# Optimization experiments

Measured on AMD Instinct MI355X. Metric: run time of the kernel, lower is better.

Reference implementation:

```python
import jax, jax.numpy as jnp
import numpy as np

DT = 0.001  # fixed dt in SimplifiedSSM.forward
LN_EPS = 1e-5


def _layernorm(x, g, b):
    m = jnp.mean(x, axis=-1, keepdims=True)
    v = jnp.mean(jnp.square(x - m), axis=-1, keepdims=True)
    return (x - m) * jax.lax.rsqrt(v + LN_EPS) * g + b


def setup_inputs() -> dict:
    key = jax.random.key(0)
    ks = jax.random.split(key, 12)
    Bn, C, H, W = 8, 1024, 32, 32
    depth, S = 4, 128
    d = C
    inp = {
        "x": jax.random.normal(ks[0], (Bn, C, H, W), dtype=jnp.float32),
        # SSM params, stacked over depth. A scaled by 0.1 for numerical stability
        # of the length-1024 recurrence (same math, tamer eigenvalues).
        "A": 0.1 * jax.random.normal(ks[1], (depth, S, S), dtype=jnp.float32),
        "Bp": jax.random.normal(ks[2], (depth, S, d), dtype=jnp.float32),
        "Cp": jax.random.normal(ks[3], (depth, d, S), dtype=jnp.float32),
        "Dp": jax.random.normal(ks[4], (depth, d), dtype=jnp.float32),
        # Linear layers (PyTorch convention: y = x @ W.T + b)
        "Wi": jax.random.normal(ks[5], (depth, d, d), dtype=jnp.float32) / np.sqrt(d),
        "bi": jax.random.normal(ks[6], (depth, d), dtype=jnp.float32) * 0.01,
        "Wo": jax.random.normal(ks[7], (depth, d, d), dtype=jnp.float32) / np.sqrt(d),
        "bo": jax.random.normal(ks[8], (depth, d), dtype=jnp.float32) * 0.01,
        # LayerNorm affine params
        "gamma": jnp.ones((depth, d), dtype=jnp.float32),
        "beta": jnp.zeros((depth, d), dtype=jnp.float32),
    }
    return inp


def reference(x, A, Bp, Cp, Dp, Wi, bi, Wo, bo, gamma, beta):
    Bn, C, H, W = x.shape
    depth, S, _ = A.shape
    # b c h w -> b (h w) c
    seq = x.reshape(Bn, C, H * W).transpose(0, 2, 1)
    eye = jnp.eye(S, dtype=x.dtype)
    for i in range(depth):
        n = _layernorm(seq, gamma[i], beta[i])
        u = n @ Wi[i].T + bi[i]                       # (B, L, d)
        A_bar = eye + DT * A[i]                       # (S, S)
        ub = jnp.einsum('bld,sd->lbs', u, DT * Bp[i]) # (L, B, S)

        def step(h, ub_t):
            h = h @ A_bar.T + ub_t
            return h, h

        h0 = jnp.zeros((Bn, S), dtype=x.dtype)
        _, hs = jax.lax.scan(step, h0, ub)            # hs: (L, B, S)
        y = jnp.einsum('lbs,ds->bld', hs, Cp[i]) + u * Dp[i]
        seq = seq + y @ Wo[i].T + bo[i]
    return seq.transpose(0, 2, 1).reshape(Bn, C, H, W)
```

## Files before the change

kernel.cpp:

```cpp
#include <hip/hip_runtime.h>
#include <stdint.h>

#define DT_STEP 0.001f
#define LN_EPS  1e-5f
#define Bn      8
#define Lseq    1024
#define Dm      1024
#define Sn      128
#define DEPTH   4
#define Mrows   (Bn * Lseq)
#define Qc      32
#define NCHUNK  (Lseq / Qc)
#define NPOW    33

typedef short bf16x8 __attribute__((ext_vector_type(8)));
typedef float f32x4  __attribute__((ext_vector_type(4)));

__device__ __forceinline__ unsigned short f2bf(float f) {
    unsigned int u = __float_as_uint(f);
    u += 0x7fffu + ((u >> 16) & 1u);
    return (unsigned short)(u >> 16);
}

#define GLOAD_LDS16(gp, lp)                                                \
    __builtin_amdgcn_global_load_lds(                                      \
        (const __attribute__((address_space(1))) unsigned int*)(gp),       \
        (__attribute__((address_space(3))) unsigned int*)(lp), 16, 0, 0)

__global__ __launch_bounds__(256) void f2bf_kernel(const float* __restrict__ src,
                                                   unsigned short* __restrict__ dst,
                                                   int n) {
    int i = (blockIdx.x * 256 + threadIdx.x) * 4;
    if (i < n) {
        float4 v = *(const float4*)(src + i);
        ushort4 o;
        o.x = f2bf(v.x); o.y = f2bf(v.y); o.z = f2bf(v.z); o.w = f2bf(v.w);
        *(ushort4*)(dst + i) = o;
    }
}

__global__ __launch_bounds__(256) void convscale_kernel(const float* __restrict__ Wo,
                                                        const float* __restrict__ Dp,
                                                        unsigned short* __restrict__ dst) {
    int z = blockIdx.y;
    int i = (blockIdx.x * 256 + threadIdx.x) * 4;
    const float* S = Wo + (size_t)z * Dm * Dm;
    const float* dp = Dp + (size_t)z * Dm;
    float4 v = *(const float4*)(S + i);
    int c = i & (Dm - 1);
    float4 d = *(const float4*)(dp + c);
    ushort4 o;
    o.x = f2bf(v.x * d.x); o.y = f2bf(v.y * d.y);
    o.z = f2bf(v.z * d.z); o.w = f2bf(v.w * d.w);
    *(ushort4*)(dst + (size_t)z * Dm * Dm + i) = o;
}

__global__ __launch_bounds__(256) void transpose_f2bf(const float* __restrict__ src,
                                                      unsigned short* __restrict__ dst,
                                                      int R, int C) {
    __shared__ float t[32][33];
    int z = blockIdx.z;
    const float* S = src + (size_t)z * R * C;
    unsigned short* D = dst + (size_t)z * R * C;
    int r0 = blockIdx.y * 32, c0 = blockIdx.x * 32;
    int tx = threadIdx.x & 31, ty = threadIdx.x >> 5;
    for (int rr = ty; rr < 32; rr += 8)
        t[rr][tx] = S[(size_t)(r0 + rr) * C + c0 + tx];
    __syncthreads();
    for (int rr = ty; rr < 32; rr += 8)
        D[(size_t)(c0 + rr) * R + r0 + tx] = f2bf(t[tx][rr]);
}

__global__ __launch_bounds__(256) void c2dt_kernel(const float* __restrict__ Bp,
                                                   const float* __restrict__ bi,
                                                   float* __restrict__ c2dt) {
    int z = blockIdx.x, s = blockIdx.y;
    int tid = threadIdx.x;
    const float* br = Bp + ((size_t)z * Sn + s) * Dm;
    const float* bb = bi + (size_t)z * Dm;
    float4 v = *(const float4*)(br + tid * 4);
    float4 w = *(const float4*)(bb + tid * 4);
    float acc = v.x * w.x + v.y * w.y + v.z * w.z + v.w * w.w;
#pragma unroll
    for (int off = 32; off > 0; off >>= 1) acc += __shfl_down(acc, off, 64);
    __shared__ float red[4];
    if ((tid & 63) == 0) red[tid >> 6] = acc;
    __syncthreads();
    if (tid == 0) c2dt[z * Sn + s] = DT_STEP * (red[0] + red[1] + red[2] + red[3]);
}

__global__ __launch_bounds__(1024) void transpose_bll(const float* __restrict__ src,
                                                      float* __restrict__ dst) {
    __shared__ float tile[32][33];
    int b  = blockIdx.z;
    int i0 = blockIdx.y * 32, j0 = blockIdx.x * 32;
    int tx = threadIdx.x, ty = threadIdx.y;
    const float* S = src + (size_t)b * Dm * Lseq;
    float*       D = dst + (size_t)b * Dm * Lseq;
    tile[ty][tx] = S[(size_t)(j0 + ty) * 1024 + i0 + tx];
    __syncthreads();
    D[(size_t)(i0 + ty) * 1024 + j0 + tx] = tile[tx][ty];
}

__global__ __launch_bounds__(256) void ln_kernel(const float* __restrict__ x,
                                                 unsigned short* __restrict__ outp,
                                                 const float* __restrict__ g,
                                                 const float* __restrict__ bta) {
    int row = blockIdx.x;
    int tid = threadIdx.x;
    const float* xr = x + (size_t)row * Dm;
    float4 v = *(const float4*)(xr + tid * 4);
    float s  = v.x + v.y + v.z + v.w;
    float ss = v.x * v.x + v.y * v.y + v.z * v.z + v.w * v.w;
#pragma unroll
    for (int off = 32; off > 0; off >>= 1) {
        s  += __shfl_down(s, off, 64);
        ss += __shfl_down(ss, off, 64);
    }
    __shared__ float red[8];
    __shared__ float mv[2];
    int wave = tid >> 6, lane = tid & 63;
    if (lane == 0) { red[wave] = s; red[4 + wave] = ss; }
    __syncthreads();
    if (tid == 0) {
        float st  = red[0] + red[1] + red[2] + red[3];
        float sst = red[4] + red[5] + red[6] + red[7];
        float mean = st / (float)Dm;
        float var  = sst / (float)Dm - mean * mean;
        mv[0] = mean;
        mv[1] = rsqrtf(var + LN_EPS);
    }
    __syncthreads();
    float mean = mv[0], rstd = mv[1];
    int c = tid * 4;
    float4 gv = *(const float4*)(g + c);
    float4 bv = *(const float4*)(bta + c);
    ushort4 o;
    o.x = f2bf((v.x - mean) * rstd * gv.x + bv.x);
    o.y = f2bf((v.y - mean) * rstd * gv.y + bv.y);
    o.z = f2bf((v.z - mean) * rstd * gv.z + bv.z);
    o.w = f2bf((v.w - mean) * rstd * gv.w + bv.w);
    *(ushort4*)(outp + (size_t)row * Dm + c) = o;
}

__global__ __launch_bounds__(512) void gemm_bk64(
    const unsigned short* __restrict__ A1, int sA1,
    const unsigned short* __restrict__ A2, int sA2, int KA1,
    const unsigned short* __restrict__ B1, int sB1,
    const unsigned short* __restrict__ B2, int sB2,
    float* __restrict__ Cf, unsigned short* __restrict__ Ch,
    const float* __restrict__ bias1, const float* __restrict__ bias2,
    int ny, int N, int K, float scale, int mode,
    long batchA, long batchB, long batchC) {
    __shared__ __align__(16) unsigned short As[1024 * 8];
    __shared__ __align__(16) unsigned short Bs[1024 * 8];
    int flat = blockIdx.x;
    int rb = flat % ny, cb = flat / ny;
    int row0 = rb * 128, col0 = cb * 128;
    int z = blockIdx.y;
    int tid  = threadIdx.x;
    int wave = tid >> 6, lane = tid & 63;
    int wm = (wave & 1) * 64, wn = (wave >> 1) * 32;
    int lr = lane & 15, lq = lane >> 4;

    int rowS[2], kclS[2], slotOff[2];
#pragma unroll
    for (int q = 0; q < 2; q++) {
        int s = tid + q * 512;
        rowS[q] = s >> 3;
        kclS[q] = (s & 7) ^ ((s >> 3) & 7);
        slotOff[q] = s * 8;
    }
    int aoff[4][2], boff[2][2];
#pragma unroll
    for (int i = 0; i < 4; i++)
#pragma unroll
        for (int h = 0; h < 2; h++) {
            int ra = wm + i * 16 + lr;
            aoff[i][h] = (ra * 8 + ((lq + 4 * h) ^ (ra & 7))) * 8;
        }
#pragma unroll
    for (int j = 0; j < 2; j++)
#pragma unroll
        for (int h = 0; h < 2; h++) {
            int rn = wn + j * 16 + lr;
            boff[j][h] = (rn * 8 + ((lq + 4 * h) ^ (rn & 7))) * 8;
        }

    const unsigned short* A1b = A1 + (size_t)z * batchA;
    const unsigned short* BfixBlk = nullptr;
    int sBfix = sB1;
    if (mode == 0) {
        if (col0 < N - 128) { BfixBlk = B1 + (size_t)col0 * sB1; sBfix = sB1; }
        else                { BfixBlk = B2;                      sBfix = sB2; }
    } else if (mode == 2) {
        BfixBlk = B1 + (size_t)z * batchB + (size_t)col0 * sB1;
        sBfix = sB1;
    }

    f32x4 acc[4][2];
#pragma unroll
    for (int i = 0; i < 4; i++)
#pragma unroll
        for (int j = 0; j < 2; j++) acc[i][j] = (f32x4){0.f, 0.f, 0.f, 0.f};

    for (int k0 = 0; k0 < K; k0 += 64) {
        const unsigned short *Ab, *Bb;
        int sa, sb, ko;
        if (mode == 1) {
            if (k0 < KA1) { Ab = A1; sa = sA1; Bb = B1 + (size_t)col0 * sB1; sb = sB1; ko = k0; }
            else          { Ab = A2; sa = sA2; Bb = B2 + (size_t)col0 * sB2; sb = sB2; ko = k0 - KA1; }
        } else {
            Ab = A1b; sa = sA1; Bb = BfixBlk; sb = sBfix; ko = k0;
        }
        const unsigned short* Abr = Ab + (size_t)row0 * sa + ko;
        const unsigned short* Bbr = Bb + ko;
        __syncthreads();
#pragma unroll
        for (int q = 0; q < 2; q++) {
            GLOAD_LDS16(Abr + (size_t)rowS[q] * sa + kclS[q] * 8, &As[slotOff[q]]);
            GLOAD_LDS16(Bbr + (size_t)rowS[q] * sb + kclS[q] * 8, &Bs[slotOff[q]]);
        }
        __syncthreads();
#pragma unroll
        for (int h = 0; h < 2; h++) {
            bf16x8 af[4], bfr[2];
#pragma unroll
            for (int i = 0; i < 4; i++) af[i]  = *(const bf16x8*)&As[aoff[i][h]];
#pragma unroll
            for (int j = 0; j < 2; j++) bfr[j] = *(const bf16x8*)&Bs[boff[j][h]];
#pragma unroll
            for (int i = 0; i < 4; i++)
#pragma unroll
                for (int j = 0; j < 2; j++)
                    acc[i][j] = __builtin_amdgcn_mfma_f32_16x16x32_bf16(af[i], bfr[j],
                                                                       acc[i][j], 0, 0, 0);
        }
    }
#pragma unroll
    for (int i = 0; i < 4; i++) {
#pragma unroll
        for (int j = 0; j < 2; j++) {
#pragma unroll
            for (int r = 0; r < 4; r++) {
                int row = row0 + wm + i * 16 + lq * 4 + r;
                int col = col0 + wn + j * 16 + lr;
                float v = acc[i][j][r];
                if (mode == 0) {
                    int nu = N - 128;
                    if (col < nu) {
                        Ch[(size_t)row * nu + col] = f2bf(v + bias1[col]);
                    } else {
                        int cc = col - nu;
                        Cf[(size_t)row * 128 + cc] = v + bias2[cc];
                    }
                } else if (mode == 1) {
                    size_t idx = (size_t)row * N + col;
                    Cf[idx] = Cf[idx] + v + bias1[col];
                } else {
                    Ch[(size_t)z * batchC + (size_t)row * N + col] = f2bf(v * scale);
                }
            }
        }
    }
}

__global__ __launch_bounds__(128) void pow_init(const float* __restrict__ Amat,
                                                float* __restrict__ Pow) {
    int i = blockIdx.x;
    int s = blockIdx.y;
    int k = threadIdx.x;
    float eye = (s == k) ? 1.f : 0.f;
    size_t base = (size_t)i * NPOW * (Sn * Sn);
    Pow[base + (size_t)s * Sn + k] = eye;
    Pow[base + (size_t)(Sn * Sn) + (size_t)s * Sn + k] =
        eye + DT_STEP * Amat[(size_t)i * Sn * Sn + (size_t)s * Sn + k];
}

__global__ __launch_bounds__(256) void pow_mul(float* __restrict__ Pow, int m, int kmax) {
    int job = blockIdx.z;
    int i  = job / kmax;
    int kk = job % kmax + 1;
    const float* Pa = Pow + ((size_t)i * NPOW + m) * (Sn * Sn);
    const float* Pb = Pow + ((size_t)i * NPOW + kk) * (Sn * Sn);
    float*       Pc = Pow + ((size_t)i * NPOW + m + kk) * (Sn * Sn);
    int r0 = blockIdx.y * 64, c0 = blockIdx.x * 32;
    __shared__ float Asl[64 * 129];
    __shared__ float Bsl[128 * 32];
    int tx = threadIdx.x, ty = threadIdx.y;
    int tid = ty * 16 + tx;
    for (int idx = tid; idx < 64 * 128; idx += 256) {
        int r = idx >> 7, cc = idx & 127;
        Asl[r * 129 + cc] = Pa[(size_t)(r0 + r) * 128 + cc];
    }
    for (int idx = tid; idx < 128 * 32; idx += 256) {
        int r = idx >> 5, cc = idx & 31;
        Bsl[r * 32 + cc] = Pb[(size_t)r * 128 + c0 + cc];
    }
    __syncthreads();
    float acc[4][2] = {{0.f,0.f},{0.f,0.f},{0.f,0.f},{0.f,0.f}};
    for (int k = 0; k < 128; k++) {
        float b0 = Bsl[k * 32 + tx * 2];
        float b1 = Bsl[k * 32 + tx * 2 + 1];
#pragma unroll
        for (int r = 0; r < 4; r++) {
            float a = Asl[(ty * 4 + r) * 129 + k];
            acc[r][0] += a * b0;
            acc[r][1] += a * b1;
        }
    }
#pragma unroll
    for (int r = 0; r < 4; r++) {
        Pc[(size_t)(r0 + ty * 4 + r) * 128 + c0 + tx * 2]     = acc[r][0];
        Pc[(size_t)(r0 + ty * 4 + r) * 128 + c0 + tx * 2 + 1] = acc[r][1];
    }
}

__global__ __launch_bounds__(128) void local_scan(const float* __restrict__ ub,
                                                  float* __restrict__ hs,
                                                  const float* __restrict__ Abar) {
    int b = blockIdx.x / NCHUNK;
    int c = blockIdx.x % NCHUNK;
    int s = threadIdx.x;
    float arow[Sn];
#pragma unroll
    for (int k = 0; k < Sn; k += 4) {
        float4 v = *(const float4*)(Abar + (size_t)s * Sn + k);
        arow[k] = v.x; arow[k + 1] = v.y; arow[k + 2] = v.z; arow[k + 3] = v.w;
    }
    __shared__ __align__(16) float hsh[Sn];
    hsh[s] = 0.f;
    __syncthreads();
    size_t base = (size_t)(b * Lseq + c * Qc) * Sn + s;
    for (int t = 0; t < Qc; t++) {
        float ut = ub[base + (size_t)t * Sn];
        float a0 = 0.f, a1 = 0.f, a2 = 0.f, a3 = 0.f;
#pragma unroll
        for (int k = 0; k < Sn; k += 16) {
            float4 h0 = *(const float4*)&hsh[k];
            float4 h1 = *(const float4*)&hsh[k + 4];
            float4 h2 = *(const float4*)&hsh[k + 8];
            float4 h3 = *(const float4*)&hsh[k + 12];
            a0 += arow[k + 0] * h0.x + arow[k + 1] * h0.y + arow[k + 2] * h0.z + arow[k + 3] * h0.w;
            a1 += arow[k + 4] * h1.x + arow[k + 5] * h1.y + arow[k + 6] * h1.z + arow[k + 7] * h1.w;
            a2 += arow[k + 8] * h2.x + arow[k + 9] * h2.y + arow[k + 10] * h2.z + arow[k + 11] * h2.w;
            a3 += arow[k + 12] * h3.x + arow[k + 13] * h3.y + arow[k + 14] * h3.z + arow[k + 15] * h3.w;
        }
        float hv = ut + (a0 + a1) + (a2 + a3);
        hs[base + (size_t)t * Sn] = hv;
        __syncthreads();
        hsh[s] = hv;
        __syncthreads();
    }
}

__global__ __launch_bounds__(128) void carry_scan(const float* __restrict__ hs,
                                                  const float* __restrict__ AQ,
                                                  float* __restrict__ carry) {
    int b = blockIdx.x;
    int s = threadIdx.x;
    float le[NCHUNK];
#pragma unroll
    for (int c = 0; c < NCHUNK; c++)
        le[c] = hs[(size_t)(b * Lseq + c * Qc + Qc - 1) * Sn + s];
    float arow[Sn];
#pragma unroll
    for (int k = 0; k < Sn; k += 4) {
        float4 v = *(const float4*)(AQ + (size_t)s * Sn + k);
        arow[k] = v.x; arow[k + 1] = v.y; arow[k + 2] = v.z; arow[k + 3] = v.w;
    }
    __shared__ __align__(16) float csh[Sn];
    csh[s] = 0.f;
    __syncthreads();
    for (int c = 0; c < NCHUNK; c++) {
        carry[((size_t)b * NCHUNK + c) * Sn + s] = csh[s];
        float a0 = 0.f, a1 = 0.f, a2 = 0.f, a3 = 0.f;
#pragma unroll
        for (int k = 0; k < Sn; k += 16) {
            float4 h0 = *(const float4*)&csh[k];
            float4 h1 = *(const float4*)&csh[k + 4];
            float4 h2 = *(const float4*)&csh[k + 8];
            float4 h3 = *(const float4*)&csh[k + 12];
            a0 += arow[k + 0] * h0.x + arow[k + 1] * h0.y + arow[k + 2] * h0.z + arow[k + 3] * h0.w;
            a1 += arow[k + 4] * h1.x + arow[k + 5] * h1.y + arow[k + 6] * h1.z + arow[k + 7] * h1.w;
            a2 += arow[k + 8] * h2.x + arow[k + 9] * h2.y + arow[k + 10] * h2.z + arow[k + 11] * h2.w;
            a3 += arow[k + 12] * h3.x + arow[k + 13] * h3.y + arow[k + 14] * h3.z + arow[k + 15] * h3.w;
        }
        float cv = le[c] + (a0 + a1) + (a2 + a3);
        __syncthreads();
        csh[s] = cv;
        __syncthreads();
    }
}

__global__ __launch_bounds__(256) void fixup_scan(const float* __restrict__ hs,
                                                  unsigned short* __restrict__ hs_bf,
                                                  const float* __restrict__ PowLayer,
                                                  const float* __restrict__ carry) {
    int t  = blockIdx.x;
    int c4 = blockIdx.y;
    const float* P = PowLayer + (size_t)(t + 1) * (Sn * Sn);
    __shared__ float Pl[Sn * 65];
    __shared__ float cl[4][Bn * Sn];
    int tid = threadIdx.x;
#pragma unroll
    for (int cc = 0; cc < 4; cc++)
        for (int idx = tid; idx < Bn * Sn; idx += 256)
            cl[cc][idx] = carry[((size_t)(idx >> 7) * NCHUNK + (c4 * 4 + cc)) * Sn + (idx & 127)];
    int s = tid & 127, bh = tid >> 7;
    float acc[4][4];
#pragma unroll
    for (int cc = 0; cc < 4; cc++)
#pragma unroll
        for (int j = 0; j < 4; j++) acc[cc][j] = 0.f;
    for (int kh = 0; kh < 2; kh++) {
        __syncthreads();
        for (int idx = tid; idx < Sn * 64; idx += 256) {
            int r = idx >> 6, kk = idx & 63;
            Pl[r * 65 + kk] = P[(size_t)r * Sn + kh * 64 + kk];
        }
        __syncthreads();
        for (int kk = 0; kk < 64; kk++) {
            float pw = Pl[s * 65 + kk];
            int kg = kh * 64 + kk;
#pragma unroll
            for (int cc = 0; cc < 4; cc++)
#pragma unroll
                for (int j = 0; j < 4; j++)
                    acc[cc][j] += pw * cl[cc][(bh * 4 + j) * Sn + kg];
        }
    }
#pragma unroll
    for (int cc = 0; cc < 4; cc++) {
        int c = c4 * 4 + cc;
#pragma unroll
        for (int j = 0; j < 4; j++) {
            int bb = bh * 4 + j;
            size_t rowi = (size_t)(bb * Lseq + c * Qc + t) * Sn + s;
            hs_bf[rowi] = f2bf(hs[rowi] + acc[cc][j]);
        }
    }
}

extern "C" void kernel_launch(void* const* d_in, const int* in_sizes, int n_in,
                              void* d_out, int out_size, void* d_ws, size_t ws_size,
                              hipStream_t stream) {
    const float* x     = (const float*)d_in[0];
    const float* Am    = (const float*)d_in[1];
    const float* Bp    = (const float*)d_in[2];
    const float* Cp    = (const float*)d_in[3];
    const float* Dp    = (const float*)d_in[4];
    const float* Wi    = (const float*)d_in[5];
    const float* bi    = (const float*)d_in[6];
    const float* Wo    = (const float*)d_in[7];
    const float* bo    = (const float*)d_in[8];
    const float* gamma = (const float*)d_in[9];
    const float* beta  = (const float*)d_in[10];
    float* out = (float*)d_out;
    (void)in_sizes; (void)n_in; (void)out_size; (void)ws_size;

    char* ws = (char*)d_ws;
    float*          seq   = (float*)(ws + (size_t)0);
    unsigned short* nbuf  = (unsigned short*)(ws + (size_t)33554432);
    unsigned short* WiTh  = (unsigned short*)(ws + (size_t)33554432);
    unsigned short* Woh   = (unsigned short*)(ws + (size_t)41943040);
    unsigned short* u     = (unsigned short*)(ws + (size_t)50331648);
    float*          ub    = (float*)(ws + (size_t)67108864);
    float*          hs    = (float*)(ws + (size_t)71303168);
    unsigned short* hs_bf = (unsigned short*)(ws + (size_t)75497472);
    float*          Pow   = (float*)(ws + (size_t)77594624);
    float*          carry = (float*)(ws + (size_t)86245376);
    unsigned short* Wih   = (unsigned short*)(ws + (size_t)86376448);
    unsigned short* Wo2h  = (unsigned short*)(ws + (size_t)94765056);
    unsigned short* Bph   = (unsigned short*)(ws + (size_t)103153664);
    unsigned short* CpTh  = (unsigned short*)(ws + (size_t)104202240);
    unsigned short* M2h   = (unsigned short*)(ws + (size_t)105250816);
    unsigned short* W3h   = (unsigned short*)(ws + (size_t)106299392);
    float*          c2dt  = (float*)(ws + (size_t)107347968);

    const long WW = (long)Dm * Dm;
    const long SW = (long)Sn * Dm;

    hipLaunchKernelGGL(f2bf_kernel, dim3(DEPTH * WW / 1024), dim3(256), 0, stream,
                       Wi, Wih, DEPTH * (int)WW);
    hipLaunchKernelGGL(f2bf_kernel, dim3(DEPTH * WW / 1024), dim3(256), 0, stream,
                       Wo, Woh, DEPTH * (int)WW);
    hipLaunchKernelGGL(f2bf_kernel, dim3(DEPTH * SW / 1024), dim3(256), 0, stream,
                       Bp, Bph, DEPTH * (int)SW);
    hipLaunchKernelGGL(convscale_kernel, dim3(WW / 1024, DEPTH), dim3(256), 0, stream,
                       Wo, Dp, Wo2h);
    hipLaunchKernelGGL(transpose_f2bf, dim3(32, 32, DEPTH), dim3(256), 0, stream,
                       Wi, WiTh, Dm, Dm);
    hipLaunchKernelGGL(transpose_f2bf, dim3(4, 32, DEPTH), dim3(256), 0, stream,
                       Cp, CpTh, Dm, Sn);
    hipLaunchKernelGGL(c2dt_kernel, dim3(DEPTH, Sn), dim3(256), 0, stream, Bp, bi, c2dt);

    hipLaunchKernelGGL(gemm_bk64, dim3(8, DEPTH), dim3(512), 0, stream,
                       Bph, Dm, (const unsigned short*)nullptr, 0, 0,
                       WiTh, Dm, (const unsigned short*)nullptr, 0,
                       (float*)nullptr, M2h, (const float*)nullptr, (const float*)nullptr,
                       1, Dm, Dm, DT_STEP, 2, SW, WW, SW);
    hipLaunchKernelGGL(gemm_bk64, dim3(8, DEPTH), dim3(512), 0, stream,
                       Woh, Dm, (const unsigned short*)nullptr, 0, 0,
                       CpTh, Dm, (const unsigned short*)nullptr, 0,
                       (float*)nullptr, W3h, (const float*)nullptr, (const float*)nullptr,
                       8, Sn, Dm, 1.f, 2, WW, SW, SW);

    hipLaunchKernelGGL(transpose_bll, dim3(32, 32, Bn), dim3(32, 32), 0, stream, x, seq);

    hipLaunchKernelGGL(pow_init, dim3(DEPTH, Sn), dim3(Sn), 0, stream, Am, Pow);
    for (int m = 1; m < Qc; m <<= 1) {
        hipLaunchKernelGGL(pow_mul, dim3(4, 2, DEPTH * m), dim3(16, 16), 0, stream,
                           Pow, m, m);
    }

    for (int i = 0; i < DEPTH; i++) {
        const unsigned short* Wi_i  = Wih  + (size_t)i * WW;
        const unsigned short* Wo2_i = Wo2h + (size_t)i * WW;
        const unsigned short* M2_i  = M2h  + (size_t)i * SW;
        const unsigned short* W3_i  = W3h  + (size_t)i * SW;
        const float* PowL = Pow + (size_t)i * NPOW * (Sn * Sn);

        hipLaunchKernelGGL(ln_kernel, dim3(Mrows), dim3(256), 0, stream,
                           seq, nbuf, gamma + i * Dm, beta + i * Dm);
        hipLaunchKernelGGL(gemm_bk64, dim3(9 * 64, 1), dim3(512), 0, stream,
                           nbuf, Dm, (const unsigned short*)nullptr, 0, 0,
                           Wi_i, Dm, M2_i, Dm,
                           ub, u, bi + i * Dm, c2dt + i * Sn,
                           64, Dm + Sn, Dm, 1.f, 0, 0, 0, 0);
        hipLaunchKernelGGL(local_scan, dim3(Bn * NCHUNK), dim3(Sn), 0, stream,
                           ub, hs, PowL + (size_t)1 * Sn * Sn);
        hipLaunchKernelGGL(carry_scan, dim3(Bn), dim3(Sn), 0, stream,
                           hs, PowL + (size_t)Qc * Sn * Sn, carry);
        hipLaunchKernelGGL(fixup_scan, dim3(Qc, NCHUNK / 4), dim3(256), 0, stream,
                           hs, hs_bf, PowL, carry);
        hipLaunchKernelGGL(gemm_bk64, dim3(8 * 64, 1), dim3(512), 0, stream,
                           hs_bf, Sn, u, Dm, Sn,
                           W3_i, Sn, Wo2_i, Dm,
                           seq, (unsigned short*)nullptr, bo + i * Dm, (const float*)nullptr,
                           64, Dm, Dm + Sn, 1.f, 1, 0, 0, 0);
    }

    hipLaunchKernelGGL(transpose_bll, dim3(32, 32, Bn), dim3(32, 32), 0, stream, seq, out);
}
```

Baseline: 812.2 us.

## Store residual stream and scan states in bf16, merge prep kernels

```diff
diff --git a/kernel.cpp b/kernel.cpp
--- a/kernel.cpp
+++ b/kernel.cpp
@@ -21,38 +21,106 @@
     u += 0x7fffu + ((u >> 16) & 1u);
     return (unsigned short)(u >> 16);
 }
+__device__ __forceinline__ float bf2f(unsigned short h) {
+    return __uint_as_float((unsigned int)h << 16);
+}
 
 #define GLOAD_LDS16(gp, lp)                                                \
     __builtin_amdgcn_global_load_lds(                                      \
         (const __attribute__((address_space(1))) unsigned int*)(gp),       \
         (__attribute__((address_space(3))) unsigned int*)(lp), 16, 0, 0)
 
-__global__ __launch_bounds__(256) void f2bf_kernel(const float* __restrict__ src,
-                                                   unsigned short* __restrict__ dst,
-                                                   int n) {
-    int i = (blockIdx.x * 256 + threadIdx.x) * 4;
-    if (i < n) {
-        float4 v = *(const float4*)(src + i);
+#define PREP_BLOCKS 18432
+__global__ __launch_bounds__(256) void prep_kernel(
+    const float* __restrict__ Wi, const float* __restrict__ Wo,
+    const float* __restrict__ Bp, const float* __restrict__ Cp,
+    const float* __restrict__ Dp, const float* __restrict__ bi,
+    const float* __restrict__ Am,
+    unsigned short* __restrict__ Wih, unsigned short* __restrict__ Woh,
+    unsigned short* __restrict__ Bph, unsigned short* __restrict__ Wo2h,
+    unsigned short* __restrict__ WiTh, unsigned short* __restrict__ CpTh,
+    float* __restrict__ c2dt, float* __restrict__ Pow) {
+    __shared__ float sm[32 * 33];
+    __shared__ float red[4];
+    int b = blockIdx.x;
+    int tid = threadIdx.x;
+    if (b < 4096) {
+        int i = (b * 256 + tid) * 4;
+        float4 v = *(const float4*)(Wi + i);
+        ushort4 o; o.x = f2bf(v.x); o.y = f2bf(v.y); o.z = f2bf(v.z); o.w = f2bf(v.w);
+        *(ushort4*)(Wih + i) = o;
+    } else if (b < 8192) {
+        int i = ((b - 4096) * 256 + tid) * 4;
+        float4 v = *(const float4*)(Wo + i);
+        ushort4 o; o.x = f2bf(v.x); o.y = f2bf(v.y); o.z = f2bf(v.z); o.w = f2bf(v.w);
+        *(ushort4*)(Woh + i) = o;
+    } else if (b < 8704) {
+        int i = ((b - 8192) * 256 + tid) * 4;
+        float4 v = *(const float4*)(Bp + i);
+        ushort4 o; o.x = f2bf(v.x); o.y = f2bf(v.y); o.z = f2bf(v.z); o.w = f2bf(v.w);
+        *(ushort4*)(Bph + i) = o;
+    } else if (b < 12800) {
+        int i = ((b - 8704) * 256 + tid) * 4;
+        int z = i >> 20;
+        int col = i & (Dm - 1);
+        float4 v = *(const float4*)(Wo + i);
+        float4 d = *(const float4*)(Dp + z * Dm + col);
         ushort4 o;
-        o.x = f2bf(v.x); o.y = f2bf(v.y); o.z = f2bf(v.z); o.w = f2bf(v.w);
-        *(ushort4*)(dst + i) = o;
-    }
-}
-
-__global__ __launch_bounds__(256) void convscale_kernel(const float* __restrict__ Wo,
-                                                        const float* __restrict__ Dp,
-                                                        unsigned short* __restrict__ dst) {
-    int z = blockIdx.y;
-    int i = (blockIdx.x * 256 + threadIdx.x) * 4;
-    const float* S = Wo + (size_t)z * Dm * Dm;
-    const float* dp = Dp + (size_t)z * Dm;
-    float4 v = *(const float4*)(S + i);
-    int c = i & (Dm - 1);
-    float4 d = *(const float4*)(dp + c);
-    ushort4 o;
-    o.x = f2bf(v.x * d.x); o.y = f2bf(v.y * d.y);
-    o.z = f2bf(v.z * d.z); o.w = f2bf(v.w * d.w);
-    *(ushort4*)(dst + (size_t)z * Dm * Dm + i) = o;
+        o.x = f2bf(v.x * d.x); o.y = f2bf(v.y * d.y);
+        o.z = f2bf(v.z * d.z); o.w = f2bf(v.w * d.w);
+        *(ushort4*)(Wo2h + i) = o;
+    } else if (b < 16896) {
+        int t = b - 12800;
+        int z = t >> 10, rem = t & 1023;
+        int bx = rem & 31, by = rem >> 5;
+        int r0 = by * 32, c0 = bx * 32;
+        const float* S = Wi + (size_t)z * Dm * Dm;
+        unsigned short* D = WiTh + (size_t)z * Dm * Dm;
+        int tx = tid & 31, ty = tid >> 5;
+        for (int rr = ty; rr < 32; rr += 8)
+            sm[rr * 33 + tx] = S[(size_t)(r0 + rr) * Dm + c0 + tx];
+        __syncthreads();
+        for (int rr = ty; rr < 32; rr += 8)
+            D[(size_t)(c0 + rr) * Dm + r0 + tx] = f2bf(sm[tx * 33 + rr]);
+    } else if (b < 17408) {
+        int t = b - 16896;
+        int z = t >> 7, rem = t & 127;
+        int bx = rem & 3, by = rem >> 2;
+        int r0 = by * 32, c0 = bx * 32;
+        const float* S = Cp + (size_t)z * Dm * Sn;
+        unsigned short* D = CpTh + (size_t)z * Dm * Sn;
+        int tx = tid & 31, ty = tid >> 5;
+        for (int rr = ty; rr < 32; rr += 8)
+            sm[rr * 33 + tx] = S[(size_t)(r0 + rr) * Sn + c0 + tx];
+        __syncthreads();
+        for (int rr = ty; rr < 32; rr += 8)
+            D[(size_t)(c0 + rr) * Dm + r0 + tx] = f2bf(sm[tx * 33 + rr]);
+    } else if (b < 17920) {
+        int t = b - 17408;
+        int z = t >> 7, s = t & 127;
+        const float* br = Bp + ((size_t)z * Sn + s) * Dm;
+        const float* bb = bi + (size_t)z * Dm;
+        float4 v = *(const float4*)(br + tid * 4);
+        float4 w = *(const float4*)(bb + tid * 4);
+        float acc = v.x * w.x + v.y * w.y + v.z * w.z + v.w * w.w;
+#pragma unroll
+        for (int off = 32; off > 0; off >>= 1) acc += __shfl_down(acc, off, 64);
+        if ((tid & 63) == 0) red[tid >> 6] = acc;
+        __syncthreads();
+        if (tid == 0) c2dt[z * Sn + s] = DT_STEP * (red[0] + red[1] + red[2] + red[3]);
+    } else {
+        int t = b - 17920;
+        int z = t >> 7, s = t & 127;
+        int k = tid & 127, half = tid >> 7;
+        size_t base = (size_t)z * NPOW * (Sn * Sn);
+        float eye = (s == k) ? 1.f : 0.f;
+        if (half == 0) {
+            Pow[base + (size_t)s * Sn + k] = eye;
+        } else {
+            Pow[base + (size_t)(Sn * Sn) + (size_t)s * Sn + k] =
+                eye + DT_STEP * Am[(size_t)z * Sn * Sn + (size_t)s * Sn + k];
+        }
+    }
 }
 
 __global__ __launch_bounds__(256) void transpose_f2bf(const float* __restrict__ src,
@@ -71,45 +139,31 @@
         D[(size_t)(c0 + rr) * R + r0 + tx] = f2bf(t[tx][rr]);
 }
 
-__global__ __launch_bounds__(256) void c2dt_kernel(const float* __restrict__ Bp,
-                                                   const float* __restrict__ bi,
-                                                   float* __restrict__ c2dt) {
-    int z = blockIdx.x, s = blockIdx.y;
-    int tid = threadIdx.x;
-    const float* br = Bp + ((size_t)z * Sn + s) * Dm;
-    const float* bb = bi + (size_t)z * Dm;
-    float4 v = *(const float4*)(br + tid * 4);
-    float4 w = *(const float4*)(bb + tid * 4);
-    float acc = v.x * w.x + v.y * w.y + v.z * w.z + v.w * w.w;
-#pragma unroll
-    for (int off = 32; off > 0; off >>= 1) acc += __shfl_down(acc, off, 64);
-    __shared__ float red[4];
-    if ((tid & 63) == 0) red[tid >> 6] = acc;
-    __syncthreads();
-    if (tid == 0) c2dt[z * Sn + s] = DT_STEP * (red[0] + red[1] + red[2] + red[3]);
-}
-
-__global__ __launch_bounds__(1024) void transpose_bll(const float* __restrict__ src,
+__global__ __launch_bounds__(256) void transpose_bf2f(const unsigned short* __restrict__ src,
                                                       float* __restrict__ dst) {
-    __shared__ float tile[32][33];
-    int b  = blockIdx.z;
-    int i0 = blockIdx.y * 32, j0 = blockIdx.x * 32;
-    int tx = threadIdx.x, ty = threadIdx.y;
-    const float* S = src + (size_t)b * Dm * Lseq;
-    float*       D = dst + (size_t)b * Dm * Lseq;
-    tile[ty][tx] = S[(size_t)(j0 + ty) * 1024 + i0 + tx];
-    __syncthreads();
-    D[(size_t)(i0 + ty) * 1024 + j0 + tx] = tile[tx][ty];
-}
-
-__global__ __launch_bounds__(256) void ln_kernel(const float* __restrict__ x,
+    __shared__ float t[32][33];
+    int z = blockIdx.z;
+    const unsigned short* S = src + (size_t)z * Dm * Lseq;
+    float* D = dst + (size_t)z * Dm * Lseq;
+    int r0 = blockIdx.y * 32, c0 = blockIdx.x * 32;
+    int tx = threadIdx.x & 31, ty = threadIdx.x >> 5;
+    for (int rr = ty; rr < 32; rr += 8)
+        t[rr][tx] = bf2f(S[(size_t)(r0 + rr) * 1024 + c0 + tx]);
+    __syncthreads();
+    for (int rr = ty; rr < 32; rr += 8)
+        D[(size_t)(c0 + rr) * 1024 + r0 + tx] = t[tx][rr];
+}
+
+__global__ __launch_bounds__(256) void ln_kernel(const unsigned short* __restrict__ x,
                                                  unsigned short* __restrict__ outp,
                                                  const float* __restrict__ g,
                                                  const float* __restrict__ bta) {
     int row = blockIdx.x;
     int tid = threadIdx.x;
-    const float* xr = x + (size_t)row * Dm;
-    float4 v = *(const float4*)(xr + tid * 4);
+    const unsigned short* xr = x + (size_t)row * Dm;
+    ushort4 hv = *(const ushort4*)(xr + tid * 4);
+    float4 v;
+    v.x = bf2f(hv.x); v.y = bf2f(hv.y); v.z = bf2f(hv.z); v.w = bf2f(hv.w);
     float s  = v.x + v.y + v.z + v.w;
     float ss = v.x * v.x + v.y * v.y + v.z * v.z + v.w * v.w;
 #pragma unroll
@@ -256,25 +310,14 @@
                     }
                 } else if (mode == 1) {
                     size_t idx = (size_t)row * N + col;
-                    Cf[idx] = Cf[idx] + v + bias1[col];
+                    float old = bf2f(Ch[idx]);
+                    Ch[idx] = f2bf(old + v + bias1[col]);
                 } else {
                     Ch[(size_t)z * batchC + (size_t)row * N + col] = f2bf(v * scale);
                 }
             }
         }
     }
-}
-
-__global__ __launch_bounds__(128) void pow_init(const float* __restrict__ Amat,
-                                                float* __restrict__ Pow) {
-    int i = blockIdx.x;
-    int s = blockIdx.y;
-    int k = threadIdx.x;
-    float eye = (s == k) ? 1.f : 0.f;
-    size_t base = (size_t)i * NPOW * (Sn * Sn);
-    Pow[base + (size_t)s * Sn + k] = eye;
-    Pow[base + (size_t)(Sn * Sn) + (size_t)s * Sn + k] =
-        eye + DT_STEP * Amat[(size_t)i * Sn * Sn + (size_t)s * Sn + k];
 }
 
 __global__ __launch_bounds__(256) void pow_mul(float* __restrict__ Pow, int m, int kmax) {
@@ -317,7 +360,8 @@
 }
 
 __global__ __launch_bounds__(128) void local_scan(const float* __restrict__ ub,
-                                                  float* __restrict__ hs,
+                                                  unsigned short* __restrict__ hs_bf,
+                                                  float* __restrict__ ends,
                                                   const float* __restrict__ Abar) {
     int b = blockIdx.x / NCHUNK;
     int c = blockIdx.x % NCHUNK;
@@ -332,6 +376,7 @@
     hsh[s] = 0.f;
     __syncthreads();
     size_t base = (size_t)(b * Lseq + c * Qc) * Sn + s;
+    float hv = 0.f;
     for (int t = 0; t < Qc; t++) {
         float ut = ub[base + (size_t)t * Sn];
         float a0 = 0.f, a1 = 0.f, a2 = 0.f, a3 = 0.f;
@@ -346,15 +391,16 @@
             a2 += arow[k + 8] * h2.x + arow[k + 9] * h2.y + arow[k + 10] * h2.z + arow[k + 11] * h2.w;
             a3 += arow[k + 12] * h3.x + arow[k + 13] * h3.y + arow[k + 14] * h3.z + arow[k + 15] * h3.w;
         }
-        float hv = ut + (a0 + a1) + (a2 + a3);
-        hs[base + (size_t)t * Sn] = hv;
+        hv = ut + (a0 + a1) + (a2 + a3);
+        hs_bf[base + (size_t)t * Sn] = f2bf(hv);
         __syncthreads();
         hsh[s] = hv;
         __syncthreads();
     }
-}
-
-__global__ __launch_bounds__(128) void carry_scan(const float* __restrict__ hs,
+    ends[((size_t)b * NCHUNK + c) * Sn + s] = hv;
+}
+
+__global__ __launch_bounds__(128) void carry_scan(const float* __restrict__ ends,
                                                   const float* __restrict__ AQ,
                                                   float* __restrict__ carry) {
     int b = blockIdx.x;
@@ -362,7 +408,7 @@
     float le[NCHUNK];
 #pragma unroll
     for (int c = 0; c < NCHUNK; c++)
-        le[c] = hs[(size_t)(b * Lseq + c * Qc + Qc - 1) * Sn + s];
+        le[c] = ends[((size_t)b * NCHUNK + c) * Sn + s];
     float arow[Sn];
 #pragma unroll
     for (int k = 0; k < Sn; k += 4) {
@@ -393,8 +439,7 @@
     }
 }
 
-__global__ __launch_bounds__(256) void fixup_scan(const float* __restrict__ hs,
-                                                  unsigned short* __restrict__ hs_bf,
+__global__ __launch_bounds__(256) void fixup_scan(unsigned short* __restrict__ hs_bf,
                                                   const float* __restrict__ PowLayer,
                                                   const float* __restrict__ carry) {
     int t  = blockIdx.x;
@@ -437,7 +482,7 @@
         for (int j = 0; j < 4; j++) {
             int bb = bh * 4 + j;
             size_t rowi = (size_t)(bb * Lseq + c * Qc + t) * Sn + s;
-            hs_bf[rowi] = f2bf(hs[rowi] + acc[cc][j]);
+            hs_bf[rowi] = f2bf(bf2f(hs_bf[rowi]) + acc[cc][j]);
         }
     }
 }
@@ -460,40 +505,30 @@
     (void)in_sizes; (void)n_in; (void)out_size; (void)ws_size;
 
     char* ws = (char*)d_ws;
-    float*          seq   = (float*)(ws + (size_t)0);
-    unsigned short* nbuf  = (unsigned short*)(ws + (size_t)33554432);
-    unsigned short* WiTh  = (unsigned short*)(ws + (size_t)33554432);
-    unsigned short* Woh   = (unsigned short*)(ws + (size_t)41943040);
-    unsigned short* u     = (unsigned short*)(ws + (size_t)50331648);
-    float*          ub    = (float*)(ws + (size_t)67108864);
-    float*          hs    = (float*)(ws + (size_t)71303168);
-    unsigned short* hs_bf = (unsigned short*)(ws + (size_t)75497472);
-    float*          Pow   = (float*)(ws + (size_t)77594624);
-    float*          carry = (float*)(ws + (size_t)86245376);
-    unsigned short* Wih   = (unsigned short*)(ws + (size_t)86376448);
-    unsigned short* Wo2h  = (unsigned short*)(ws + (size_t)94765056);
-    unsigned short* Bph   = (unsigned short*)(ws + (size_t)103153664);
-    unsigned short* CpTh  = (unsigned short*)(ws + (size_t)104202240);
-    unsigned short* M2h   = (unsigned short*)(ws + (size_t)105250816);
-    unsigned short* W3h   = (unsigned short*)(ws + (size_t)106299392);
-    float*          c2dt  = (float*)(ws + (size_t)107347968);
+    unsigned short* seqh  = (unsigned short*)(ws + (size_t)0);
+    unsigned short* nbuf  = (unsigned short*)(ws + (size_t)16777216);
+    unsigned short* WiTh  = (unsigned short*)(ws + (size_t)16777216);
+    unsigned short* Woh   = (unsigned short*)(ws + (size_t)25165824);
+    unsigned short* u     = (unsigned short*)(ws + (size_t)33554432);
+    float*          ub    = (float*)(ws + (size_t)50331648);
+    unsigned short* hs_bf = (unsigned short*)(ws + (size_t)54525952);
+    float*          ends  = (float*)(ws + (size_t)56623104);
+    float*          Pow   = (float*)(ws + (size_t)56754176);
+    float*          carry = (float*)(ws + (size_t)65404928);
+    unsigned short* Wih   = (unsigned short*)(ws + (size_t)65536000);
+    unsigned short* Wo2h  = (unsigned short*)(ws + (size_t)73924608);
+    unsigned short* Bph   = (unsigned short*)(ws + (size_t)82313216);
+    unsigned short* CpTh  = (unsigned short*)(ws + (size_t)83361792);
+    unsigned short* M2h   = (unsigned short*)(ws + (size_t)84410368);
+    unsigned short* W3h   = (unsigned short*)(ws + (size_t)85458944);
+    float*          c2dt  = (float*)(ws + (size_t)86507520);
 
     const long WW = (long)Dm * Dm;
     const long SW = (long)Sn * Dm;
 
-    hipLaunchKernelGGL(f2bf_kernel, dim3(DEPTH * WW / 1024), dim3(256), 0, stream,
-                       Wi, Wih, DEPTH * (int)WW);
-    hipLaunchKernelGGL(f2bf_kernel, dim3(DEPTH * WW / 1024), dim3(256), 0, stream,
-                       Wo, Woh, DEPTH * (int)WW);
-    hipLaunchKernelGGL(f2bf_kernel, dim3(DEPTH * SW / 1024), dim3(256), 0, stream,
-                       Bp, Bph, DEPTH * (int)SW);
-    hipLaunchKernelGGL(convscale_kernel, dim3(WW / 1024, DEPTH), dim3(256), 0, stream,
-                       Wo, Dp, Wo2h);
-    hipLaunchKernelGGL(transpose_f2bf, dim3(32, 32, DEPTH), dim3(256), 0, stream,
-                       Wi, WiTh, Dm, Dm);
-    hipLaunchKernelGGL(transpose_f2bf, dim3(4, 32, DEPTH), dim3(256), 0, stream,
-                       Cp, CpTh, Dm, Sn);
-    hipLaunchKernelGGL(c2dt_kernel, dim3(DEPTH, Sn), dim3(256), 0, stream, Bp, bi, c2dt);
+    hipLaunchKernelGGL(prep_kernel, dim3(PREP_BLOCKS), dim3(256), 0, stream,
+                       Wi, Wo, Bp, Cp, Dp, bi, Am,
+                       Wih, Woh, Bph, Wo2h, WiTh, CpTh, c2dt, Pow);
 
     hipLaunchKernelGGL(gemm_bk64, dim3(8, DEPTH), dim3(512), 0, stream,
                        Bph, Dm, (const unsigned short*)nullptr, 0, 0,
@@ -506,9 +541,9 @@
                        (float*)nullptr, W3h, (const float*)nullptr, (const float*)nullptr,
                        8, Sn, Dm, 1.f, 2, WW, SW, SW);
 
-    hipLaunchKernelGGL(transpose_bll, dim3(32, 32, Bn), dim3(32, 32), 0, stream, x, seq);
-
-    hipLaunchKernelGGL(pow_init, dim3(DEPTH, Sn), dim3(Sn), 0, stream, Am, Pow);
+    hipLaunchKernelGGL(transpose_f2bf, dim3(32, 32, Bn), dim3(256), 0, stream,
+                       x, seqh, Dm, Lseq);
+
     for (int m = 1; m < Qc; m <<= 1) {
         hipLaunchKernelGGL(pow_mul, dim3(4, 2, DEPTH * m), dim3(16, 16), 0, stream,
                            Pow, m, m);
@@ -522,24 +557,24 @@
         const float* PowL = Pow + (size_t)i * NPOW * (Sn * Sn);
 
         hipLaunchKernelGGL(ln_kernel, dim3(Mrows), dim3(256), 0, stream,
-                           seq, nbuf, gamma + i * Dm, beta + i * Dm);
+                           seqh, nbuf, gamma + i * Dm, beta + i * Dm);
         hipLaunchKernelGGL(gemm_bk64, dim3(9 * 64, 1), dim3(512), 0, stream,
                            nbuf, Dm, (const unsigned short*)nullptr, 0, 0,
                            Wi_i, Dm, M2_i, Dm,
                            ub, u, bi + i * Dm, c2dt + i * Sn,
                            64, Dm + Sn, Dm, 1.f, 0, 0, 0, 0);
         hipLaunchKernelGGL(local_scan, dim3(Bn * NCHUNK), dim3(Sn), 0, stream,
-                           ub, hs, PowL + (size_t)1 * Sn * Sn);
+                           ub, hs_bf, ends, PowL + (size_t)1 * Sn * Sn);
         hipLaunchKernelGGL(carry_scan, dim3(Bn), dim3(Sn), 0, stream,
-                           hs, PowL + (size_t)Qc * Sn * Sn, carry);
+                           ends, PowL + (size_t)Qc * Sn * Sn, carry);
         hipLaunchKernelGGL(fixup_scan, dim3(Qc, NCHUNK / 4), dim3(256), 0, stream,
-                           hs, hs_bf, PowL, carry);
+                           hs_bf, PowL, carry);
         hipLaunchKernelGGL(gemm_bk64, dim3(8 * 64, 1), dim3(512), 0, stream,
                            hs_bf, Sn, u, Dm, Sn,
                            W3_i, Sn, Wo2_i, Dm,
-                           seq, (unsigned short*)nullptr, bo + i * Dm, (const float*)nullptr,
+                           (float*)nullptr, seqh, bo + i * Dm, (const float*)nullptr,
                            64, Dm, Dm + Sn, 1.f, 1, 0, 0, 0);
     }
 
-    hipLaunchKernelGGL(transpose_bll, dim3(32, 32, Bn), dim3(32, 32), 0, stream, seq, out);
-}
+    hipLaunchKernelGGL(transpose_bf2f, dim3(32, 32, Bn), dim3(256), 0, stream, seqh, out);
+}
```

After: 825.9 us. No clear change (+1.7%).
